# Kernel optimization log

Measured on AMD Instinct MI355X. Metric: run time of the kernel, lower is better.

Reference implementation:

```python
import jax, jax.numpy as jnp
import numpy as np

N_P, N_S, N_D = 100000, 2000, 3
C_P, C_S, C_D = 128, 64, 16
HID, HEADS, NCLS = 128, 4, 3
E_HAS, E_BEL, E_SIM = 300000, 100000, 400000
BN_EPS = 1e-5

def _segment_softmax(alpha, seg, num_segments):
    # PyG-style softmax over destination segments: exp(a - max) / (sum + 1e-16)
    amax = jax.ops.segment_max(alpha, seg, num_segments=num_segments)
    amax = jnp.where(jnp.isfinite(amax), amax, 0.0)
    e = jnp.exp(alpha - amax[seg])
    denom = jax.ops.segment_sum(e, seg, num_segments=num_segments)
    return e / (denom[seg] + 1e-16)

def _han_edge(x_src, x_dst, ei, a_src, a_dst, num_dst):
    # x_*: [N, H, D]; a_*: [H, D]; ei: [2, E]. GAT-style per-edge-type attention.
    s, d = ei[0], ei[1]
    al_s = jnp.einsum('nhd,hd->nh', x_src, a_src)
    al_d = jnp.einsum('nhd,hd->nh', x_dst, a_dst)
    alpha = jax.nn.leaky_relu(al_s[s] + al_d[d], 0.2)      # [E, H]
    w = _segment_softmax(alpha, d, num_dst)
    msg = x_src[s] * w[:, :, None]                          # [E, H, D]
    out = jax.ops.segment_sum(msg, d, num_segments=num_dst)
    H, D = a_src.shape
    return jax.nn.relu(out.reshape(num_dst, H * D))

def _han_layer(x_p, x_s, x_d, ei_has, ei_bel, ei_sim,
               wp, bp, ws, bs, wd, bd,
               a_sh, a_dh, a_sb, a_db, a_ss, a_ds, heads, out_ch):
    D = out_ch // heads
    hp = (x_p @ wp.T + bp).reshape(-1, heads, D)
    hs = (x_s @ ws.T + bs).reshape(-1, heads, D)
    hd = (x_d @ wd.T + bd).reshape(-1, heads, D)
    out_s = _han_edge(hp, hs, ei_has, a_sh, a_dh, hs.shape[0])
    out_d = _han_edge(hp, hd, ei_bel, a_sb, a_db, hd.shape[0])
    out_p = _han_edge(hp, hp, ei_sim, a_ss, a_ds, hp.shape[0])
    # Semantic attention (group): each dst type receives exactly one metapath
    # here, so softmax over a single score is identically 1 and fusion is the
    # identity -- the semantic q/k_lin params have no numerical effect.
    return out_p, out_s, out_d

def reference(x_patient, x_symptom, x_dosha, ei_has, ei_bel, ei_sim,
              w1_patient, b1_patient, w1_symptom, b1_symptom, w1_dosha, b1_dosha,
              a1_src_has, a1_dst_has, a1_src_bel, a1_dst_bel, a1_src_sim, a1_dst_sim,
              bn_w, bn_b, bn_mean, bn_var,
              w2_patient, b2_patient, w2_symptom, b2_symptom, w2_dosha, b2_dosha,
              a2_src_has, a2_dst_has, a2_src_bel, a2_dst_bel, a2_src_sim, a2_dst_sim):
    op, os_, od = _han_layer(x_patient, x_symptom, x_dosha, ei_has, ei_bel, ei_sim,
                             w1_patient, b1_patient, w1_symptom, b1_symptom, w1_dosha, b1_dosha,
                             a1_src_has, a1_dst_has, a1_src_bel, a1_dst_bel,
                             a1_src_sim, a1_dst_sim, HEADS, HID)
    # eval-mode BatchNorm1d shared across node types, then ELU (dropout = id in eval)
    inv = bn_w / jnp.sqrt(bn_var + BN_EPS)
    bn_elu = lambda v: jax.nn.elu((v - bn_mean) * inv + bn_b)
    op, os_, od = bn_elu(op), bn_elu(os_), bn_elu(od)
    op2, _, _ = _han_layer(op, os_, od, ei_has, ei_bel, ei_sim,
                           w2_patient, b2_patient, w2_symptom, b2_symptom, w2_dosha, b2_dosha,
                           a2_src_has, a2_dst_has, a2_src_bel, a2_dst_bel,
                           a2_src_sim, a2_dst_sim, 1, NCLS)
    return jax.nn.log_softmax(op2, axis=1)

def setup_inputs():
    key = jax.random.key(0)
    ks = list(jax.random.split(key, 32))
    nrm = lambda k, shp, s: jax.random.normal(k, shp, jnp.float32) * s
    ri = lambda k, n, hi: jax.random.randint(k, (n,), 0, hi, dtype=jnp.int32)
    D1 = HID // HEADS
    inp = {}
    inp['x_patient'] = nrm(ks[0], (N_P, C_P), 1.0)
    inp['x_symptom'] = nrm(ks[1], (N_S, C_S), 1.0)
    inp['x_dosha'] = nrm(ks[2], (N_D, C_D), 1.0)
    inp['ei_has'] = jnp.stack([ri(ks[3], E_HAS, N_P), ri(ks[4], E_HAS, N_S)])
    inp['ei_bel'] = jnp.stack([ri(ks[5], E_BEL, N_P), ri(ks[6], E_BEL, N_D)])
    inp['ei_sim'] = jnp.stack([ri(ks[7], E_SIM, N_P), ri(ks[8], E_SIM, N_P)])
    inp['w1_patient'] = nrm(ks[9], (HID, C_P), 0.05); inp['b1_patient'] = jnp.zeros(HID)
    inp['w1_symptom'] = nrm(ks[10], (HID, C_S), 0.05); inp['b1_symptom'] = jnp.zeros(HID)
    inp['w1_dosha'] = nrm(ks[11], (HID, C_D), 0.05); inp['b1_dosha'] = jnp.zeros(HID)
    inp['a1_src_has'] = nrm(ks[12], (HEADS, D1), 0.1); inp['a1_dst_has'] = nrm(ks[13], (HEADS, D1), 0.1)
    inp['a1_src_bel'] = nrm(ks[14], (HEADS, D1), 0.1); inp['a1_dst_bel'] = nrm(ks[15], (HEADS, D1), 0.1)
    inp['a1_src_sim'] = nrm(ks[16], (HEADS, D1), 0.1); inp['a1_dst_sim'] = nrm(ks[17], (HEADS, D1), 0.1)
    inp['bn_w'] = jnp.ones(HID); inp['bn_b'] = jnp.zeros(HID)
    inp['bn_mean'] = jnp.zeros(HID); inp['bn_var'] = jnp.ones(HID)
    inp['w2_patient'] = nrm(ks[18], (NCLS, HID), 0.05); inp['b2_patient'] = jnp.zeros(NCLS)
    inp['w2_symptom'] = nrm(ks[19], (NCLS, HID), 0.05); inp['b2_symptom'] = jnp.zeros(NCLS)
    inp['w2_dosha'] = nrm(ks[20], (NCLS, HID), 0.05); inp['b2_dosha'] = jnp.zeros(NCLS)
    inp['a2_src_has'] = nrm(ks[21], (1, NCLS), 0.1); inp['a2_dst_has'] = nrm(ks[22], (1, NCLS), 0.1)
    inp['a2_src_bel'] = nrm(ks[23], (1, NCLS), 0.1); inp['a2_dst_bel'] = nrm(ks[24], (1, NCLS), 0.1)
    inp['a2_src_sim'] = nrm(ks[25], (1, NCLS), 0.1); inp['a2_dst_sim'] = nrm(ks[26], (1, NCLS), 0.1)
    return inp
```

## Files before the change

kernel.cpp:

```cpp
#include <hip/hip_runtime.h>
#include <hip/hip_bf16.h>

typedef float f32x4 __attribute__((ext_vector_type(4)));
typedef unsigned short u16x4 __attribute__((ext_vector_type(4)));
typedef unsigned short u16x8 __attribute__((ext_vector_type(8)));
typedef short bf16x8 __attribute__((ext_vector_type(8)));

#define HID 128
#define RT  4

__device__ __forceinline__ float b2f(unsigned short u) {
    return __uint_as_float(((unsigned int)u) << 16);
}
__device__ __forceinline__ unsigned short f2b(float f) {
    unsigned int u = __float_as_uint(f);
    unsigned int r = (u + 0x7FFFu + ((u >> 16) & 1u)) >> 16;
    return (unsigned short)r;
}

__device__ __forceinline__ bool detect_f32(const unsigned short* xp) {
    int sane = 0;
#pragma unroll
    for (int i = 0; i < 16; ++i) {
        int ex = (xp[2 * i] >> 7) & 0xFF;
        sane += (ex >= 120 && ex <= 130);
    }
    return sane < 8;
}
__device__ __forceinline__ bool detect_i64(const int* ei) {
    return (ei[1] | ei[3] | ei[5] | ei[7]) == 0;
}
__device__ __forceinline__ float ldf(const unsigned short* p, long i, bool f32) {
    return f32 ? ((const float*)p)[i] : b2f(p[i]);
}
__device__ __forceinline__ f32x4 ld4(const unsigned short* p, int c0, bool f32) {
    if (f32) return *(const f32x4*)((const float*)p + c0);
    u16x4 q = *(const u16x4*)(p + c0);
    return (f32x4){b2f(q[0]), b2f(q[1]), b2f(q[2]), b2f(q[3])};
}
__device__ __forceinline__ int ei_at(const int* ei, long idx, bool i64) {
    return i64 ? ei[2 * idx] : ei[idx];
}
__device__ __forceinline__ float lrelu(float a) {
    return a > 0.f ? a : 0.2f * a;
}

__global__ __launch_bounds__(256) void gemm1_deg_k(
    const unsigned short* __restrict__ x,
    const unsigned short* __restrict__ w,
    const unsigned short* __restrict__ bias,
    const unsigned short* __restrict__ a1s,
    const unsigned short* __restrict__ a1d,
    unsigned short* __restrict__ hp,
    float* __restrict__ al_s, float* __restrict__ al_d, int n_rows,
    const int* __restrict__ ei, int E, int* __restrict__ deg, int gb)
{
    if ((int)blockIdx.x >= gb) {
        const bool i64 = detect_i64(ei);
        int e = ((int)blockIdx.x - gb) * 256 + threadIdx.x;
        if (e < E) atomicAdd(&deg[ei_at(ei, (long)E + e, i64)], 1);
        return;
    }

    const bool f32m = detect_f32(x);
    const int wave  = threadIdx.x >> 6;
    const int lane  = threadIdx.x & 63;
    const int nhalf = wave & 1;
    const int rtile = wave >> 1;
    const int m     = lane & 15;
    const int quad  = lane >> 4;

    bf16x8 wfrag[4][4];
#pragma unroll
    for (int ks = 0; ks < 4; ++ks)
#pragma unroll
        for (int nt = 0; nt < 4; ++nt) {
            int col = nhalf * 64 + nt * 16 + m;
            if (!f32m) {
                wfrag[ks][nt] = *(const bf16x8*)(w + (long)col * HID + ks * 32 + quad * 8);
            } else {
                const float* wf = (const float*)w;
#pragma unroll
                for (int j = 0; j < 8; ++j)
                    wfrag[ks][nt][j] = (short)f2b(wf[(long)col * HID + ks * 32 + quad * 8 + j]);
            }
        }

    const long base = (long)blockIdx.x * (32 * RT);

#pragma unroll
    for (int tt = 0; tt < RT; ++tt) {
        const long row0 = base + tt * 32 + rtile * 16;
        if (row0 >= n_rows) break;
        const long row = row0 + m;

        bf16x8 afrag[4];
        {
            long arow = row < n_rows ? row : n_rows - 1;
            if (!f32m) {
#pragma unroll
                for (int ks = 0; ks < 4; ++ks)
                    afrag[ks] = *(const bf16x8*)(x + arow * HID + ks * 32 + quad * 8);
            } else {
                const float* xf = (const float*)x;
#pragma unroll
                for (int ks = 0; ks < 4; ++ks)
#pragma unroll
                    for (int j = 0; j < 8; ++j)
                        afrag[ks][j] = (short)f2b(xf[arow * HID + ks * 32 + quad * 8 + j]);
            }
        }

        f32x4 acc[4];
#pragma unroll
        for (int nt = 0; nt < 4; ++nt) acc[nt] = (f32x4){0.f, 0.f, 0.f, 0.f};
#pragma unroll
        for (int nt = 0; nt < 4; ++nt)
#pragma unroll
            for (int ks = 0; ks < 4; ++ks)
                acc[nt] = __builtin_amdgcn_mfma_f32_16x16x32_bf16(
                    wfrag[ks][nt], afrag[ks], acc[nt], 0, 0, 0);

        float als_p[2] = {0.f, 0.f}, ald_p[2] = {0.f, 0.f};
#pragma unroll
        for (int nt = 0; nt < 4; ++nt) {
            const int c0 = nhalf * 64 + nt * 16 + quad * 4;
            const f32x4 bb  = ld4(bias, c0, f32m);
            const f32x4 as4 = ld4(a1s,  c0, f32m);
            const f32x4 ad4 = ld4(a1d,  c0, f32m);
            float v0 = acc[nt][0] + bb[0];
            float v1 = acc[nt][1] + bb[1];
            float v2 = acc[nt][2] + bb[2];
            float v3 = acc[nt][3] + bb[3];
            if (row < n_rows) {
                u16x4 st = {f2b(v0), f2b(v1), f2b(v2), f2b(v3)};
                *(u16x4*)(hp + row * HID + c0) = st;
            }
            const int hl = nt >> 1;
            als_p[hl] += v0 * as4[0] + v1 * as4[1] + v2 * as4[2] + v3 * as4[3];
            ald_p[hl] += v0 * ad4[0] + v1 * ad4[1] + v2 * ad4[2] + v3 * ad4[3];
        }
#pragma unroll
        for (int off = 16; off < 64; off <<= 1) {
            als_p[0] += __shfl_xor(als_p[0], off);
            als_p[1] += __shfl_xor(als_p[1], off);
            ald_p[0] += __shfl_xor(ald_p[0], off);
            ald_p[1] += __shfl_xor(ald_p[1], off);
        }
        if (quad == 0 && row < n_rows) {
            const int hb = nhalf * 2;
            al_s[row * 4 + hb + 0] = als_p[0];
            al_s[row * 4 + hb + 1] = als_p[1];
            al_d[row * 4 + hb + 0] = ald_p[0];
            al_d[row * 4 + hb + 1] = ald_p[1];
        }
    }
}

__global__ void base_k(const int* __restrict__ deg, int n,
                       int* __restrict__ rowptr, int* __restrict__ cursor,
                       int* __restrict__ gctr)
{
    int g = blockIdx.x * 256 + threadIdx.x;
    int lane = threadIdx.x & 63;
    int dg = (g < n) ? deg[g] : 0;
    int val = dg;
#pragma unroll
    for (int off = 1; off < 64; off <<= 1) {
        int y = __shfl_up(val, off);
        if (lane >= off) val += y;
    }
    int wtot = __shfl(val, 63);
    int base = 0;
    if (lane == 63) base = atomicAdd(gctr, wtot);
    base = __shfl(base, 63);
    int start = base + val - dg;
    if (g < n) { rowptr[g] = start; cursor[g] = start; }
}

__global__ void scatter_k(const int* __restrict__ ei, int E,
                          int* __restrict__ cursor, int* __restrict__ csrc)
{
    const bool i64 = detect_i64(ei);
    int e = blockIdx.x * 256 + threadIdx.x;
    if (e >= E) return;
    int s = ei_at(ei, e, i64);
    int d = ei_at(ei, (long)E + e, i64);
    int pos = atomicAdd(&cursor[d], 1);
    csrc[pos] = s;
}

__global__ __launch_bounds__(256) void msg1_fused_k(
    const int* __restrict__ rowptr, const int* __restrict__ deg,
    const int* __restrict__ csrc,
    const unsigned short* __restrict__ hp,
    const float* __restrict__ al_s, const float* __restrict__ al_d,
    const unsigned short* __restrict__ bn_w, const unsigned short* __restrict__ bn_b,
    const unsigned short* __restrict__ bn_m, const unsigned short* __restrict__ bn_v,
    const unsigned short* __restrict__ w2,   const unsigned short* __restrict__ b2,
    const unsigned short* __restrict__ a2s,  const unsigned short* __restrict__ a2d,
    const unsigned short* __restrict__ xp,
    float* __restrict__ hp2, float* __restrict__ al2s, float* __restrict__ al2d,
    int n_p)
{
    const bool f32m = detect_f32(xp);
    __shared__ float s_inv[128], s_mu[128], s_beta[128];
    __shared__ float s_w2[3][128];
    __shared__ float s_scal[9];
    {
        int t = threadIdx.x;
        if (t < 128) {
            float bw = ldf(bn_w, t, f32m), bv = ldf(bn_v, t, f32m);
            s_inv[t]  = bw / sqrtf(bv + 1e-5f);
            s_mu[t]   = ldf(bn_m, t, f32m);
            s_beta[t] = ldf(bn_b, t, f32m);
            s_w2[0][t] = ldf(w2, 0 * HID + t, f32m);
            s_w2[1][t] = ldf(w2, 1 * HID + t, f32m);
            s_w2[2][t] = ldf(w2, 2 * HID + t, f32m);
        } else if (t < 131) {
            int k = t - 128;
            s_scal[k]     = ldf(b2, k, f32m);
            s_scal[3 + k] = ldf(a2s, k, f32m);
            s_scal[6 + k] = ldf(a2d, k, f32m);
        }
    }
    __syncthreads();

    const int lt = threadIdx.x & 15;
    const int d  = blockIdx.x * 16 + (threadIdx.x >> 4);
    if (d >= n_p) return;
    const int h = lt >> 2;
    const float ald = al_d[(long)d * 4 + h];
    const int beg = rowptr[d], end = beg + deg[d];

    float dsum = 0.f;
    float acc[8] = {0.f,0.f,0.f,0.f,0.f,0.f,0.f,0.f};
    int p = beg;
    for (; p + 4 <= end; p += 4) {
        int s0 = csrc[p + 0], s1 = csrc[p + 1], s2 = csrc[p + 2], s3 = csrc[p + 3];
        float a0 = al_s[(long)s0 * 4 + h];
        float a1 = al_s[(long)s1 * 4 + h];
        float a2 = al_s[(long)s2 * 4 + h];
        float a3 = al_s[(long)s3 * 4 + h];
        u16x8 v0 = *(const u16x8*)(hp + (long)s0 * HID + lt * 8);
        u16x8 v1 = *(const u16x8*)(hp + (long)s1 * HID + lt * 8);
        u16x8 v2 = *(const u16x8*)(hp + (long)s2 * HID + lt * 8);
        u16x8 v3 = *(const u16x8*)(hp + (long)s3 * HID + lt * 8);
        float w0 = __expf(lrelu(a0 + ald));
        float w1 = __expf(lrelu(a1 + ald));
        float w2_ = __expf(lrelu(a2 + ald));
        float w3 = __expf(lrelu(a3 + ald));
        dsum += (w0 + w1) + (w2_ + w3);
#pragma unroll
        for (int k = 0; k < 8; ++k)
            acc[k] += b2f(v0[k]) * w0 + b2f(v1[k]) * w1
                    + b2f(v2[k]) * w2_ + b2f(v3[k]) * w3;
    }
    for (; p < end; ++p) {
        int s = csrc[p];
        float w = __expf(lrelu(al_s[(long)s * 4 + h] + ald));
        u16x8 v = *(const u16x8*)(hp + (long)s * HID + lt * 8);
        dsum += w;
#pragma unroll
        for (int k = 0; k < 8; ++k)
            acc[k] += b2f(v[k]) * w;
    }

    const float r = 1.f / (dsum + 1e-16f);
    float p0 = 0.f, p1 = 0.f, p2 = 0.f;
#pragma unroll
    for (int k = 0; k < 8; ++k) {
        int j = lt * 8 + k;
        float v = acc[k] * r;
        v = v > 0.f ? v : 0.f;
        v = (v - s_mu[j]) * s_inv[j] + s_beta[j];
        v = v > 0.f ? v : (__expf(v) - 1.f);
        p0 += v * s_w2[0][j];
        p1 += v * s_w2[1][j];
        p2 += v * s_w2[2][j];
    }
#pragma unroll
    for (int msk = 8; msk; msk >>= 1) {
        p0 += __shfl_xor(p0, msk);
        p1 += __shfl_xor(p1, msk);
        p2 += __shfl_xor(p2, msk);
    }
    if (lt == 0) {
        p0 += s_scal[0]; p1 += s_scal[1]; p2 += s_scal[2];
        *(f32x4*)(hp2 + (long)d * 4) = (f32x4){p0, p1, p2, 0.f};
        al2s[d] = p0 * s_scal[3] + p1 * s_scal[4] + p2 * s_scal[5];
        al2d[d] = p0 * s_scal[6] + p1 * s_scal[7] + p2 * s_scal[8];
    }
}

__global__ __launch_bounds__(256) void l2final_k(
    const int* __restrict__ rowptr, const int* __restrict__ deg,
    const int* __restrict__ csrc,
    const float* __restrict__ hp2,
    const float* __restrict__ al2s, const float* __restrict__ al2d,
    const unsigned short* __restrict__ xp,
    void* __restrict__ out, int n_p)
{
    const bool f32m = detect_f32(xp);
    const int t  = blockIdx.x * 256 + threadIdx.x;
    const int d  = t >> 2;
    const int sl = t & 3;
    if (d >= n_p) return;
    const int beg = rowptr[d], end = beg + deg[d];
    const float ald = al2d[d];

    float a0s = 0.f, a1s = 0.f, a2s_ = 0.f, ds = 0.f;
    for (int p = beg + sl; p < end; p += 4) {
        int s = csrc[p];
        float w = __expf(lrelu(al2s[s] + ald));
        f32x4 hv = *(const f32x4*)(hp2 + (long)s * 4);
        ds += w;
        a0s += hv[0] * w; a1s += hv[1] * w; a2s_ += hv[2] * w;
    }
#pragma unroll
    for (int off = 1; off < 4; off <<= 1) {
        ds  += __shfl_xor(ds, off);
        a0s += __shfl_xor(a0s, off);
        a1s += __shfl_xor(a1s, off);
        a2s_ += __shfl_xor(a2s_, off);
    }
    if (sl != 0) return;

    const float r = 1.f / (ds + 1e-16f);
    float v0 = fmaxf(a0s * r, 0.f);
    float v1 = fmaxf(a1s * r, 0.f);
    float v2 = fmaxf(a2s_ * r, 0.f);
    float m = fmaxf(v0, fmaxf(v1, v2));
    float lse = m + __logf(__expf(v0 - m) + __expf(v1 - m) + __expf(v2 - m));
    if (f32m) {
        float* o = (float*)out;
        o[(long)d * 3 + 0] = v0 - lse;
        o[(long)d * 3 + 1] = v1 - lse;
        o[(long)d * 3 + 2] = v2 - lse;
    } else {
        __hip_bfloat16* o = (__hip_bfloat16*)out;
        o[(long)d * 3 + 0] = __float2bfloat16(v0 - lse);
        o[(long)d * 3 + 1] = __float2bfloat16(v1 - lse);
        o[(long)d * 3 + 2] = __float2bfloat16(v2 - lse);
    }
}

extern "C" void kernel_launch(void* const* d_in, const int* in_sizes, int n_in,
                              void* d_out, int out_size, void* d_ws, size_t ws_size,
                              hipStream_t stream)
{
    const unsigned short* x_p = (const unsigned short*)d_in[0];
    const int*            ei  = (const int*)d_in[5];
    const unsigned short* w1p = (const unsigned short*)d_in[6];
    const unsigned short* b1p = (const unsigned short*)d_in[7];
    const unsigned short* a1s = (const unsigned short*)d_in[16];
    const unsigned short* a1d = (const unsigned short*)d_in[17];
    const unsigned short* bnw = (const unsigned short*)d_in[18];
    const unsigned short* bnb = (const unsigned short*)d_in[19];
    const unsigned short* bnm = (const unsigned short*)d_in[20];
    const unsigned short* bnv = (const unsigned short*)d_in[21];
    const unsigned short* w2p = (const unsigned short*)d_in[22];
    const unsigned short* b2p = (const unsigned short*)d_in[23];
    const unsigned short* a2s = (const unsigned short*)d_in[32];
    const unsigned short* a2d = (const unsigned short*)d_in[33];

    const int n_p   = in_sizes[0] / HID;
    const int e_sim = in_sizes[5] / 2;

    float* ws = (float*)d_ws;
    size_t o = 0;
    int* gctr = (int*)(ws + o);                       o += 4;
    int* deg  = (int*)(ws + o);                       o += (size_t)n_p;
    size_t zlen = o;
    int* rowptr = (int*)(ws + o);                     o += (size_t)n_p;
    int* cursor = (int*)(ws + o);                     o += (size_t)n_p;
    int* csrc   = (int*)(ws + o);                     o += (size_t)e_sim;
    unsigned short* hp = (unsigned short*)(ws + o);   o += (size_t)n_p * HID / 2;
    float* al_s = ws + o;                             o += (size_t)n_p * 4;
    float* al_d = ws + o;                             o += (size_t)n_p * 4;
    float* hp2  = ws + o;                             o += (size_t)n_p * 4;
    float* al2s = ws + o;                             o += (size_t)n_p;
    float* al2d = ws + o;                             o += (size_t)n_p;

    hipMemsetAsync((void*)ws, 0, zlen * sizeof(float), stream);

    const int gb = (n_p + 32 * RT - 1) / (32 * RT);
    const int db = (e_sim + 255) / 256;
    gemm1_deg_k<<<gb + db, 256, 0, stream>>>(
        x_p, w1p, b1p, a1s, a1d, hp, al_s, al_d, n_p, ei, e_sim, deg, gb);

    base_k<<<(n_p + 255) / 256, 256, 0, stream>>>(deg, n_p, rowptr, cursor, gctr);
    scatter_k<<<(e_sim + 255) / 256, 256, 0, stream>>>(ei, e_sim, cursor, csrc);

    msg1_fused_k<<<(n_p + 15) / 16, 256, 0, stream>>>(rowptr, deg, csrc, hp, al_s, al_d,
                                                      bnw, bnb, bnm, bnv, w2p, b2p,
                                                      a2s, a2d, x_p,
                                                      hp2, al2s, al2d, n_p);

    l2final_k<<<((long)n_p * 4 + 255) / 256, 256, 0, stream>>>(
        rowptr, deg, csrc, hp2, al2s, al2d, x_p, d_out, n_p);
}
```

Baseline: 290.1 us.

## Split degree count from GEMM, batch edge atomics, pack al2s into hp2

The degree count moves out of the fused GEMM launch into its own kernel, and each thread now handles four edges with their loads issued before the atomics, in both the degree and scatter kernels. The GEMM runs after CSR construction. The layer-2 source attention scalar is packed into the unused fourth slot of the hp2 vector, so the final aggregation reads one 16-byte vector per edge instead of a separate gather. This trades away the overlap of degree counting with the GEMM for better memory-level parallelism and fewer random gathers.

```diff
diff --git a/kernel.cpp b/kernel.cpp
--- a/kernel.cpp
+++ b/kernel.cpp
@@ -45,23 +45,15 @@
     return a > 0.f ? a : 0.2f * a;
 }
 
-__global__ __launch_bounds__(256) void gemm1_deg_k(
+__global__ __launch_bounds__(256) void gemm1_k(
     const unsigned short* __restrict__ x,
     const unsigned short* __restrict__ w,
     const unsigned short* __restrict__ bias,
     const unsigned short* __restrict__ a1s,
     const unsigned short* __restrict__ a1d,
     unsigned short* __restrict__ hp,
-    float* __restrict__ al_s, float* __restrict__ al_d, int n_rows,
-    const int* __restrict__ ei, int E, int* __restrict__ deg, int gb)
-{
-    if ((int)blockIdx.x >= gb) {
-        const bool i64 = detect_i64(ei);
-        int e = ((int)blockIdx.x - gb) * 256 + threadIdx.x;
-        if (e < E) atomicAdd(&deg[ei_at(ei, (long)E + e, i64)], 1);
-        return;
-    }
-
+    float* __restrict__ al_s, float* __restrict__ al_d, int n_rows)
+{
     const bool f32m = detect_f32(x);
     const int wave  = threadIdx.x >> 6;
     const int lane  = threadIdx.x & 63;
@@ -157,6 +149,23 @@
     }
 }
 
+__global__ __launch_bounds__(256) void deg_k(const int* __restrict__ ei, int E,
+                                             int* __restrict__ deg, int nth)
+{
+    const bool i64 = detect_i64(ei);
+    const int idx = blockIdx.x * 256 + threadIdx.x;
+    int d[4]; bool v[4];
+#pragma unroll
+    for (int k = 0; k < 4; ++k) {
+        int e = idx + k * nth;
+        v[k] = e < E;
+        d[k] = v[k] ? ei_at(ei, (long)E + e, i64) : 0;
+    }
+#pragma unroll
+    for (int k = 0; k < 4; ++k)
+        if (v[k]) atomicAdd(&deg[d[k]], 1);
+}
+
 __global__ void base_k(const int* __restrict__ deg, int n,
                        int* __restrict__ rowptr, int* __restrict__ cursor,
                        int* __restrict__ gctr)
@@ -178,16 +187,28 @@
     if (g < n) { rowptr[g] = start; cursor[g] = start; }
 }
 
-__global__ void scatter_k(const int* __restrict__ ei, int E,
-                          int* __restrict__ cursor, int* __restrict__ csrc)
+__global__ __launch_bounds__(256) void scatter_k(const int* __restrict__ ei, int E,
+                                                 int* __restrict__ cursor,
+                                                 int* __restrict__ csrc, int nth)
 {
     const bool i64 = detect_i64(ei);
-    int e = blockIdx.x * 256 + threadIdx.x;
-    if (e >= E) return;
-    int s = ei_at(ei, e, i64);
-    int d = ei_at(ei, (long)E + e, i64);
-    int pos = atomicAdd(&cursor[d], 1);
-    csrc[pos] = s;
+    const int idx = blockIdx.x * 256 + threadIdx.x;
+    int s[4], d[4]; bool v[4];
+#pragma unroll
+    for (int k = 0; k < 4; ++k) {
+        int e = idx + k * nth;
+        v[k] = e < E;
+        if (v[k]) {
+            s[k] = ei_at(ei, e, i64);
+            d[k] = ei_at(ei, (long)E + e, i64);
+        }
+    }
+#pragma unroll
+    for (int k = 0; k < 4; ++k)
+        if (v[k]) {
+            int pos = atomicAdd(&cursor[d[k]], 1);
+            csrc[pos] = s[k];
+        }
 }
 
 __global__ __launch_bounds__(256) void msg1_fused_k(
@@ -200,7 +221,7 @@
     const unsigned short* __restrict__ w2,   const unsigned short* __restrict__ b2,
     const unsigned short* __restrict__ a2s,  const unsigned short* __restrict__ a2d,
     const unsigned short* __restrict__ xp,
-    float* __restrict__ hp2, float* __restrict__ al2s, float* __restrict__ al2d,
+    float* __restrict__ hp2, float* __restrict__ al2d,
     int n_p)
 {
     const bool f32m = detect_f32(xp);
@@ -287,8 +308,8 @@
     }
     if (lt == 0) {
         p0 += s_scal[0]; p1 += s_scal[1]; p2 += s_scal[2];
-        *(f32x4*)(hp2 + (long)d * 4) = (f32x4){p0, p1, p2, 0.f};
-        al2s[d] = p0 * s_scal[3] + p1 * s_scal[4] + p2 * s_scal[5];
+        float a2sv = p0 * s_scal[3] + p1 * s_scal[4] + p2 * s_scal[5];
+        *(f32x4*)(hp2 + (long)d * 4) = (f32x4){p0, p1, p2, a2sv};
         al2d[d] = p0 * s_scal[6] + p1 * s_scal[7] + p2 * s_scal[8];
     }
 }
@@ -297,7 +318,7 @@
     const int* __restrict__ rowptr, const int* __restrict__ deg,
     const int* __restrict__ csrc,
     const float* __restrict__ hp2,
-    const float* __restrict__ al2s, const float* __restrict__ al2d,
+    const float* __restrict__ al2d,
     const unsigned short* __restrict__ xp,
     void* __restrict__ out, int n_p)
 {
@@ -312,8 +333,8 @@
     float a0s = 0.f, a1s = 0.f, a2s_ = 0.f, ds = 0.f;
     for (int p = beg + sl; p < end; p += 4) {
         int s = csrc[p];
-        float w = __expf(lrelu(al2s[s] + ald));
         f32x4 hv = *(const f32x4*)(hp2 + (long)s * 4);
+        float w = __expf(lrelu(hv[3] + ald));
         ds += w;
         a0s += hv[0] * w; a1s += hv[1] * w; a2s_ += hv[2] * w;
     }
@@ -379,24 +400,23 @@
     float* al_s = ws + o;                             o += (size_t)n_p * 4;
     float* al_d = ws + o;                             o += (size_t)n_p * 4;
     float* hp2  = ws + o;                             o += (size_t)n_p * 4;
-    float* al2s = ws + o;                             o += (size_t)n_p;
     float* al2d = ws + o;                             o += (size_t)n_p;
 
     hipMemsetAsync((void*)ws, 0, zlen * sizeof(float), stream);
 
-    const int gb = (n_p + 32 * RT - 1) / (32 * RT);
-    const int db = (e_sim + 255) / 256;
-    gemm1_deg_k<<<gb + db, 256, 0, stream>>>(
-        x_p, w1p, b1p, a1s, a1d, hp, al_s, al_d, n_p, ei, e_sim, deg, gb);
-
+    const int csr_blocks = (e_sim + 4 * 256 - 1) / (4 * 256);
+    const int csr_nth    = csr_blocks * 256;
+    deg_k<<<csr_blocks, 256, 0, stream>>>(ei, e_sim, deg, csr_nth);
     base_k<<<(n_p + 255) / 256, 256, 0, stream>>>(deg, n_p, rowptr, cursor, gctr);
-    scatter_k<<<(e_sim + 255) / 256, 256, 0, stream>>>(ei, e_sim, cursor, csrc);
-
+    scatter_k<<<csr_blocks, 256, 0, stream>>>(ei, e_sim, cursor, csrc, csr_nth);
+
+    gemm1_k<<<(n_p + 32 * RT - 1) / (32 * RT), 256, 0, stream>>>(
+        x_p, w1p, b1p, a1s, a1d, hp, al_s, al_d, n_p);
     msg1_fused_k<<<(n_p + 15) / 16, 256, 0, stream>>>(rowptr, deg, csrc, hp, al_s, al_d,
                                                       bnw, bnb, bnm, bnv, w2p, b2p,
                                                       a2s, a2d, x_p,
-                                                      hp2, al2s, al2d, n_p);
+                                                      hp2, al2d, n_p);
 
     l2final_k<<<((long)n_p * 4 + 255) / 256, 256, 0, stream>>>(
-        rowptr, deg, csrc, hp2, al2s, al2d, x_p, d_out, n_p);
-}
+        rowptr, deg, csrc, hp2, al2d, x_p, d_out, n_p);
+}
```

New measurement: 294.6 us. About the same (+1.5%).
